# Kernel tuning notes

Measured on AMD Instinct MI355X. Metric: run time of the kernel, lower is better.

## Reference

```python
import jax, jax.numpy as jnp
import numpy as np

N_NODES = 50000
D_MODEL = 128
N_EDGES = 600000
HIDDEN = 128
EDGE_FEAT = 2 * D_MODEL + 2  # 258


def setup_inputs() -> dict:
    key = jax.random.key(0)
    k = jax.random.split(key, 8)
    H = jax.random.normal(k[0], (N_NODES, D_MODEL), dtype=jnp.float32)
    edge_index = jax.random.randint(k[1], (2, N_EDGES), 0, N_NODES, dtype=jnp.int64)
    S_e = jax.random.uniform(k[2], (N_EDGES,), dtype=jnp.float32)
    F_e = jax.random.uniform(k[3], (N_EDGES,), dtype=jnp.float32)
    W1 = jax.random.normal(k[4], (EDGE_FEAT, HIDDEN), dtype=jnp.float32) * (1.0 / np.sqrt(EDGE_FEAT))
    b1 = jnp.zeros((HIDDEN,), dtype=jnp.float32)
    W2 = jax.random.normal(k[5], (HIDDEN, 1), dtype=jnp.float32) * (1.0 / np.sqrt(HIDDEN))
    b2 = jnp.zeros((1,), dtype=jnp.float32)
    return {"H": H, "edge_index": edge_index, "S_e": S_e, "F_e": F_e,
            "W1": W1, "b1": b1, "W2": W2, "b2": b2}


def reference(H, edge_index, S_e, F_e, W1, b1, W2, b2):
    # Gather endpoint node features: [E, D]
    H_u = H[edge_index[0]]
    H_v = H[edge_index[1]]
    H_diff = jnp.abs(H_u - H_v)
    H_prod = H_u * H_v
    # [E, 2D+2]
    edge_features = jnp.concatenate(
        [H_diff, H_prod, S_e[:, None], F_e[:, None]], axis=1)
    # 2-layer MLP with SiLU (dropout is identity in eval mode)
    h = jax.nn.silu(edge_features @ W1 + b1)
    a_e = (h @ W2 + b2)[:, 0]  # [E]
    return a_e
```

## Files before the change

kernel.cpp:

```cpp
#include <hip/hip_runtime.h>


typedef _Float16       half8   __attribute__((ext_vector_type(8)));
typedef _Float16       half4v  __attribute__((ext_vector_type(4)));
typedef unsigned short ushort8 __attribute__((ext_vector_type(8)));
typedef float          f32x4   __attribute__((ext_vector_type(4)));

#define NSEG    8

__device__ __forceinline__ float silu_f(float x) {
    return x / (1.0f + __expf(-x));
}


__global__ __launch_bounds__(256)
void cvt_zero_kernel(const float* __restrict__ H, _Float16* __restrict__ Hh,
                     int n4, int* __restrict__ zp, int nz) {
    int i = blockIdx.x * blockDim.x + threadIdx.x;
    if (i < nz) zp[i] = 0;
    if (i < n4) {
        const float4 f = ((const float4*)H)[i];
        half4v h;
        h[0] = (_Float16)f.x; h[1] = (_Float16)f.y;
        h[2] = (_Float16)f.z; h[3] = (_Float16)f.w;
        ((half4v*)Hh)[i] = h;
    }
}

__device__ __forceinline__ void canon(int u, int v, int& a, int& b) {
    const int sw = (u ^ v) & 1;
    a = sw ? v : u;
    b = sw ? u : v;
}

__global__ __launch_bounds__(256)
void hist_kernel(const int* __restrict__ eidx, int* __restrict__ hist,
                 int E, int ASZ, int BBINS) {
    int e = blockIdx.x * blockDim.x + threadIdx.x;
    if (e < E) {
        int a, b;
        canon(eidx[e], eidx[E + e], a, b);
        atomicAdd(&hist[(a / ASZ) * BBINS + (b >> 3)], 1);
    }
}

__global__ __launch_bounds__(256)
void scan1_kernel(int* __restrict__ hist, int* __restrict__ bsum, int NB) {
    __shared__ int s[256];
    const int t = threadIdx.x;
    const int i = blockIdx.x * 256 + t;
    const int v = (i < NB) ? hist[i] : 0;
    s[t] = v;
    __syncthreads();
    for (int off = 1; off < 256; off <<= 1) {
        const int x = (t >= off) ? s[t - off] : 0;
        __syncthreads();
        s[t] += x;
        __syncthreads();
    }
    if (i < NB) hist[i] = s[t] - v;
    if (t == 255) bsum[blockIdx.x] = s[255];
}

__global__ __launch_bounds__(256)
void scan2_kernel(int* __restrict__ bsum, int nb1,
                  const int* __restrict__ hist, int* __restrict__ vbs,
                  int BBINS, int E) {
    __shared__ int s[256];
    const int t = threadIdx.x;
    const int v = (t < nb1) ? bsum[t] : 0;
    s[t] = v;
    __syncthreads();
    for (int off = 1; off < 256; off <<= 1) {
        const int x = (t >= off) ? s[t - off] : 0;
        __syncthreads();
        s[t] += x;
        __syncthreads();
    }
    if (t < nb1) bsum[t] = s[t] - v;
    __syncthreads();
    if (t < NSEG) {
        const int idx = t * BBINS;
        vbs[t] = hist[idx] + bsum[idx >> 8];
    } else if (t == NSEG) {
        vbs[NSEG] = E;
    }
}

__global__ __launch_bounds__(256)
void scatter_kernel(const int* __restrict__ eidx, const float* __restrict__ Se,
                    const float* __restrict__ Fe, int* __restrict__ ofs,
                    const int* __restrict__ bsum,
                    int4* __restrict__ recs, int E, int ASZ, int BBINS) {
    int e = blockIdx.x * blockDim.x + threadIdx.x;
    if (e < E) {
        int a, b;
        canon(eidx[e], eidx[E + e], a, b);
        const int key = (a / ASZ) * BBINS + (b >> 3);
        const int pos = atomicAdd(&ofs[key], 1) + bsum[key >> 8];
        _Float16 sh = (_Float16)Se[e];
        _Float16 fh = (_Float16)Fe[e];
        unsigned pk = (unsigned)*(unsigned short*)&sh
                    | ((unsigned)*(unsigned short*)&fh << 16);
        recs[pos] = make_int4(a, b, e, (int)pk);
    }
}


__device__ __forceinline__ void stage_w1(const float* __restrict__ W1,
                                         _Float16* __restrict__ w1t, int tid) {
    const int n = tid & 127;
    const int g = tid >> 7;
    #pragma unroll
    for (int i = 0; i < 8; ++i) {
        const int kb = g + (i << 2);
        half8 tmp;
        #pragma unroll
        for (int j = 0; j < 8; ++j) {
            const int kp = (kb << 3) + j;
            const int c  = kp >> 5;
            const int r5 = kp & 31;
            const int qq = r5 >> 3;
            const int jj = r5 & 7;
            const int d  = ((c >> 1) << 5) + (qq << 3) + ((c & 1) << 2) + (jj >> 1);
            const int src = ((jj & 1) << 7) + d;
            tmp[j] = (_Float16)W1[src * 128 + n];
        }
        *(half8*)&w1t[n * 256 + ((kb ^ (n & 7)) << 3)] = tmp;
    }
}


__global__ __launch_bounds__(512, 4)
void edgegate_seg(const _Float16* __restrict__ Hh,
                  const int4*  __restrict__ recs,
                  const int*   __restrict__ vbs,
                  int*         __restrict__ ctr,
                  const float* __restrict__ W1,
                  const float* __restrict__ b1,
                  const float* __restrict__ W2,
                  const float* __restrict__ b2,
                  float*       __restrict__ out)
{
    __shared__ _Float16 w1t[128 * 256];
    __shared__ int tkt[2];
    const int tid = threadIdx.x;
    stage_w1(W1, w1t, tid);

    int xcd;
    asm volatile("s_getreg_b32 %0, hwreg(HW_REG_XCC_ID)" : "=s"(xcd));
    xcd &= (NSEG - 1);

    __syncthreads();

    const int lane = tid & 63;
    const int wave = tid >> 6;
    const int q    = lane >> 4;
    const int cb   = lane & 15;
    const int swz  = cb & 7;

    int p = 0;
    for (int sidx = 0; sidx < NSEG; ++sidx) {
        const int seg = (xcd + sidx) & (NSEG - 1);
        const int vs  = vbs[seg];
        const int ve  = vbs[seg + 1];
        const int ner = ve - vs;
        if (ner <= 0) continue;
        const int Tt = (ner + 255) >> 8;

        while (true) {
            if (tid == 0) tkt[p] = atomicAdd(&ctr[seg], 1);
            __syncthreads();
            const int t0 = tkt[p];
            p ^= 1;
            if (t0 >= Tt) break;

            const int ebase = vs + (t0 << 8) + (wave << 5);

            int a_[2], b_[2], oe_[2];
            float Sf_[2], Ff_[2];
            const _Float16 *up[2], *vp[2];
            #pragma unroll
            for (int g = 0; g < 2; ++g) {
                const int e = min(ebase + (g << 4) + cb, ve - 1);
                const int4 r = recs[e];
                a_[g] = r.x; b_[g] = r.y; oe_[g] = r.z;
                const unsigned pk = (unsigned)r.w;
                const unsigned short sl = (unsigned short)(pk & 0xFFFF);
                const unsigned short fl = (unsigned short)(pk >> 16);
                Sf_[g] = (float)*(const _Float16*)&sl;
                Ff_[g] = (float)*(const _Float16*)&fl;
                up[g] = Hh + (size_t)a_[g] * 128;
                vp[g] = Hh + (size_t)b_[g] * 128;
            }

            f32x4 acc[2][8];
            #pragma unroll
            for (int g = 0; g < 2; ++g)
                #pragma unroll
                for (int t = 0; t < 8; ++t) acc[g][t] = (f32x4){0.f, 0.f, 0.f, 0.f};

            #pragma unroll
            for (int c8 = 0; c8 < 4; ++c8) {
                half8 ae[2], ao[2];
                #pragma unroll
                for (int g = 0; g < 2; ++g) {
                    const half8 u8 = *(const half8*)(up[g] + (c8 << 5) + (q << 3));
                    const half8 v8 = *(const half8*)(vp[g] + (c8 << 5) + (q << 3));
                    half8 d8 = u8 - v8;
                    ushort8 du = *(ushort8*)&d8;
                    du = du & (unsigned short)0x7FFF;
                    const half8 da = *(half8*)&du;
                    const half8 p8 = u8 * v8;
                    ae[g][0]=da[0]; ae[g][1]=p8[0]; ae[g][2]=da[1]; ae[g][3]=p8[1];
                    ae[g][4]=da[2]; ae[g][5]=p8[2]; ae[g][6]=da[3]; ae[g][7]=p8[3];
                    ao[g][0]=da[4]; ao[g][1]=p8[4]; ao[g][2]=da[5]; ao[g][3]=p8[5];
                    ao[g][4]=da[6]; ao[g][5]=p8[6]; ao[g][6]=da[7]; ao[g][7]=p8[7];
                }

                const int kb0 = (((c8 << 1) + 0) * 4 + q) ^ swz;
                const int kb1 = (((c8 << 1) + 1) * 4 + q) ^ swz;
                #pragma unroll
                for (int t = 0; t < 8; ++t) {
                    const half8 b0 = *(const half8*)&w1t[((t << 4) + cb) * 256 + (kb0 << 3)];
                    acc[0][t] = __builtin_amdgcn_mfma_f32_16x16x32_f16(ae[0], b0, acc[0][t], 0, 0, 0);
                    acc[1][t] = __builtin_amdgcn_mfma_f32_16x16x32_f16(ae[1], b0, acc[1][t], 0, 0, 0);
                }
                #pragma unroll
                for (int t = 0; t < 8; ++t) {
                    const half8 b1f = *(const half8*)&w1t[((t << 4) + cb) * 256 + (kb1 << 3)];
                    acc[0][t] = __builtin_amdgcn_mfma_f32_16x16x32_f16(ao[0], b1f, acc[0][t], 0, 0, 0);
                    acc[1][t] = __builtin_amdgcn_mfma_f32_16x16x32_f16(ao[1], b1f, acc[1][t], 0, 0, 0);
                }
            }

            #pragma unroll
            for (int g = 0; g < 2; ++g) {
                float s_r[4], f_r[4]; int oe_r[4];
                #pragma unroll
                for (int rr = 0; rr < 4; ++rr) {
                    const int src = (q << 2) + rr;
                    s_r[rr]  = __shfl(Sf_[g], src);
                    f_r[rr]  = __shfl(Ff_[g], src);
                    oe_r[rr] = __shfl(oe_[g], src);
                }

                float rs[4] = {0.f, 0.f, 0.f, 0.f};
                #pragma unroll
                for (int t = 0; t < 8; ++t) {
                    const int col    = (t << 4) + cb;
                    const float w256 = W1[32768 + col];
                    const float w257 = W1[32896 + col];
                    const float b1c  = b1[col];
                    const float w2c  = W2[col];
                    const f32x4 av = acc[g][t];
                    #pragma unroll
                    for (int rr = 0; rr < 4; ++rr)
                        rs[rr] += silu_f(av[rr] + s_r[rr] * w256 + f_r[rr] * w257 + b1c) * w2c;
                }

                #pragma unroll
                for (int off = 1; off < 16; off <<= 1) {
                    #pragma unroll
                    for (int rr = 0; rr < 4; ++rr) rs[rr] += __shfl_xor(rs[rr], off);
                }

                if (cb == 0) {
                    const float b2v = b2[0];
                    #pragma unroll
                    for (int rr = 0; rr < 4; ++rr) {
                        const int pe = ebase + (g << 4) + (q << 2) + rr;
                        if (pe < ve) out[oe_r[rr]] = rs[rr] + b2v;
                    }
                }
            }
        }
    }
}


__global__ __launch_bounds__(512, 4)
void edgegate_fb(const float* __restrict__ H,
                 const _Float16* __restrict__ Hh,
                 const int*   __restrict__ eidx,
                 const float* __restrict__ Se,
                 const float* __restrict__ Fe,
                 const float* __restrict__ W1,
                 const float* __restrict__ b1,
                 const float* __restrict__ W2,
                 const float* __restrict__ b2,
                 float*       __restrict__ out,
                 int E, int ntiles, int useF16)
{
    __shared__ _Float16 w1t[128 * 256];
    const int tid = threadIdx.x;
    stage_w1(W1, w1t, tid);
    __syncthreads();

    const int lane = tid & 63;
    const int wave = tid >> 6;
    const int q    = lane >> 4;
    const int cb   = lane & 15;
    const int swz  = cb & 7;

    for (int tile = blockIdx.x; tile < ntiles; tile += gridDim.x) {
        const int ebase = tile * 128 + wave * 16;
        int e = ebase + cb;
        if (e >= E) e = E - 1;
        const int u = eidx[e];
        const int v = eidx[E + e];

        f32x4 acc[8];
        #pragma unroll
        for (int t = 0; t < 8; ++t) acc[t] = (f32x4){0.f, 0.f, 0.f, 0.f};

        #pragma unroll
        for (int c8 = 0; c8 < 4; ++c8) {
            half8 ae, ao;
            if (useF16) {
                const _Float16* up = Hh + (size_t)u * 128;
                const _Float16* vp = Hh + (size_t)v * 128;
                const half8 u8 = *(const half8*)(up + (c8 << 5) + (q << 3));
                const half8 v8 = *(const half8*)(vp + (c8 << 5) + (q << 3));
                half8 d8 = u8 - v8;
                ushort8 du = *(ushort8*)&d8;
                du = du & (unsigned short)0x7FFF;
                const half8 da = *(half8*)&du;
                const half8 p8 = u8 * v8;
                ae[0]=da[0]; ae[1]=p8[0]; ae[2]=da[1]; ae[3]=p8[1];
                ae[4]=da[2]; ae[5]=p8[2]; ae[6]=da[3]; ae[7]=p8[3];
                ao[0]=da[4]; ao[1]=p8[4]; ao[2]=da[5]; ao[3]=p8[5];
                ao[4]=da[6]; ao[5]=p8[6]; ao[6]=da[7]; ao[7]=p8[7];
            } else {
                const float* up = H + (size_t)u * 128;
                const float* vp = H + (size_t)v * 128;
                const float4 uu0 = *(const float4*)(up + (c8 << 5) + (q << 3));
                const float4 vv0 = *(const float4*)(vp + (c8 << 5) + (q << 3));
                const float4 uu1 = *(const float4*)(up + (c8 << 5) + (q << 3) + 4);
                const float4 vv1 = *(const float4*)(vp + (c8 << 5) + (q << 3) + 4);
                ae[0]=(_Float16)fabsf(uu0.x-vv0.x); ae[1]=(_Float16)(uu0.x*vv0.x);
                ae[2]=(_Float16)fabsf(uu0.y-vv0.y); ae[3]=(_Float16)(uu0.y*vv0.y);
                ae[4]=(_Float16)fabsf(uu0.z-vv0.z); ae[5]=(_Float16)(uu0.z*vv0.z);
                ae[6]=(_Float16)fabsf(uu0.w-vv0.w); ae[7]=(_Float16)(uu0.w*vv0.w);
                ao[0]=(_Float16)fabsf(uu1.x-vv1.x); ao[1]=(_Float16)(uu1.x*vv1.x);
                ao[2]=(_Float16)fabsf(uu1.y-vv1.y); ao[3]=(_Float16)(uu1.y*vv1.y);
                ao[4]=(_Float16)fabsf(uu1.z-vv1.z); ao[5]=(_Float16)(uu1.z*vv1.z);
                ao[6]=(_Float16)fabsf(uu1.w-vv1.w); ao[7]=(_Float16)(uu1.w*vv1.w);
            }
            const int kb0 = (((c8 << 1) + 0) * 4 + q) ^ swz;
            const int kb1 = (((c8 << 1) + 1) * 4 + q) ^ swz;
            #pragma unroll
            for (int t = 0; t < 8; ++t) {
                const half8 b0 = *(const half8*)&w1t[((t << 4) + cb) * 256 + (kb0 << 3)];
                acc[t] = __builtin_amdgcn_mfma_f32_16x16x32_f16(ae, b0, acc[t], 0, 0, 0);
            }
            #pragma unroll
            for (int t = 0; t < 8; ++t) {
                const half8 b1f = *(const half8*)&w1t[((t << 4) + cb) * 256 + (kb1 << 3)];
                acc[t] = __builtin_amdgcn_mfma_f32_16x16x32_f16(ao, b1f, acc[t], 0, 0, 0);
            }
        }

        const int e0  = ebase + (q << 2);
        const int e0c = (e0 + 3 < E) ? e0 : (E - 4);
        const float4 s4 = *(const float4*)(Se + e0c);
        const float4 f4 = *(const float4*)(Fe + e0c);

        float rs0 = 0.f, rs1 = 0.f, rs2 = 0.f, rs3 = 0.f;
        #pragma unroll
        for (int t = 0; t < 8; ++t) {
            const int col    = (t << 4) + cb;
            const float w256 = W1[32768 + col];
            const float w257 = W1[32896 + col];
            const float b1c  = b1[col];
            const float w2c  = W2[col];
            const f32x4 av = acc[t];
            rs0 += silu_f(av[0] + s4.x * w256 + f4.x * w257 + b1c) * w2c;
            rs1 += silu_f(av[1] + s4.y * w256 + f4.y * w257 + b1c) * w2c;
            rs2 += silu_f(av[2] + s4.z * w256 + f4.z * w257 + b1c) * w2c;
            rs3 += silu_f(av[3] + s4.w * w256 + f4.w * w257 + b1c) * w2c;
        }
        #pragma unroll
        for (int off = 1; off < 16; off <<= 1) {
            rs0 += __shfl_xor(rs0, off);
            rs1 += __shfl_xor(rs1, off);
            rs2 += __shfl_xor(rs2, off);
            rs3 += __shfl_xor(rs3, off);
        }
        if (cb == 0 && e0 < E) {
            const float b2v = b2[0];
            out[e0]     = rs0 + b2v;
            out[e0 + 1] = rs1 + b2v;
            out[e0 + 2] = rs2 + b2v;
            out[e0 + 3] = rs3 + b2v;
        }
    }
}


static inline size_t align256(size_t x) { return (x + 255) & ~(size_t)255; }

extern "C" void kernel_launch(void* const* d_in, const int* in_sizes, int n_in,
                              void* d_out, int out_size, void* d_ws, size_t ws_size,
                              hipStream_t stream)
{
    const float* H    = (const float*)d_in[0];
    const int*   eidx = (const int*)  d_in[1];
    const float* Se   = (const float*)d_in[2];
    const float* Fe   = (const float*)d_in[3];
    const float* W1   = (const float*)d_in[4];
    const float* b1   = (const float*)d_in[5];
    const float* W2   = (const float*)d_in[6];
    const float* b2   = (const float*)d_in[7];
    float* out = (float*)d_out;

    const int nH     = in_sizes[0];
    const int nNodes = nH / 128;
    const int E      = in_sizes[2];
    const int ntiles = (E + 127) / 128;

    const int ASZ   = (nNodes + NSEG - 1) / NSEG;
    const int BBINS = (nNodes + 7) >> 3;
    const int NB    = NSEG * BBINS;
    const int nb1   = (NB + 255) / 256;

    const size_t hhB    = (size_t)nH * sizeof(_Float16);
    const size_t off_g  = align256(hhB);
    const size_t off_bs = align256(off_g + (size_t)(NB + 8) * 4);
    const size_t off_vb = align256(off_bs + 256 * 4);
    const size_t off_r  = align256(off_vb + 16 * 4);
    const size_t need   = off_r + (size_t)E * sizeof(int4);

    if (ws_size >= need && nb1 <= 256) {
        _Float16* Hh   = (_Float16*)((char*)d_ws);
        int*      hist = (int*)     ((char*)d_ws + off_g);
        int*      ctr  = hist + NB;
        int*      bsum = (int*)     ((char*)d_ws + off_bs);
        int*      vbs  = (int*)     ((char*)d_ws + off_vb);
        int4*     recs = (int4*)    ((char*)d_ws + off_r);

        const int n4 = nH / 4;
        hipLaunchKernelGGL(cvt_zero_kernel, dim3((n4 + 255) / 256), dim3(256), 0,
                           stream, H, Hh, n4, hist, NB + 8);
        hipLaunchKernelGGL(hist_kernel, dim3((E + 255) / 256), dim3(256), 0, stream,
                           eidx, hist, E, ASZ, BBINS);
        hipLaunchKernelGGL(scan1_kernel, dim3(nb1), dim3(256), 0, stream,
                           hist, bsum, NB);
        hipLaunchKernelGGL(scan2_kernel, dim3(1), dim3(256), 0, stream,
                           bsum, nb1, hist, vbs, BBINS, E);
        hipLaunchKernelGGL(scatter_kernel, dim3((E + 255) / 256), dim3(256), 0, stream,
                           eidx, Se, Fe, hist, bsum, recs, E, ASZ, BBINS);

        hipLaunchKernelGGL(edgegate_seg, dim3(512), dim3(512), 0, stream,
                           Hh, recs, vbs, ctr, W1, b1, W2, b2, out);
    } else if (ws_size >= hhB) {
        _Float16* Hh = (_Float16*)d_ws;
        const int n4 = nH / 4;
        const int grid = (512 < ntiles) ? 512 : ntiles;
        hipLaunchKernelGGL(cvt_zero_kernel, dim3((n4 + 255) / 256), dim3(256), 0,
                           stream, H, Hh, n4, (int*)nullptr, 0);
        hipLaunchKernelGGL(edgegate_fb, dim3(grid), dim3(512), 0, stream,
                           H, Hh, eidx, Se, Fe, W1, b1, W2, b2, out, E, ntiles, 1);
    } else {
        const int grid = (512 < ntiles) ? 512 : ntiles;
        hipLaunchKernelGGL(edgegate_fb, dim3(grid), dim3(512), 0, stream,
                           H, (const _Float16*)nullptr, eidx, Se, Fe, W1, b1, W2, b2,
                           out, E, ntiles, 0);
    }
}
```

Baseline: 307.4 us.

## Fuse preprocessing and edge MLP into one cooperative megakernel with grid syncs

Replaces the six-kernel pipeline (convert/zero, histogram, two scans, scatter, edge MLP) with a single cooperative kernel that separates the phases with grid.sync, removing the per-launch overhead and the gaps between small kernels. The scan is reworked into a per-block chunk scan plus a block-0 scan of the block sums. The edge tile per wave shrinks from 32 to 16 edges, which lowers register pressure but gives less reuse of W1 fragments. The W1 staging permutation is simplified so the MFMA operands no longer need interleaving shuffles. Grid syncs add their own latency, and the old pipeline remains as a fallback if the cooperative launch fails.

```diff
diff --git a/kernel.cpp b/kernel.cpp
--- a/kernel.cpp
+++ b/kernel.cpp
@@ -1,4 +1,7 @@
 #include <hip/hip_runtime.h>
+#include <hip/hip_cooperative_groups.h>
+
+namespace cg = cooperative_groups;
 
 
 typedef _Float16       half8   __attribute__((ext_vector_type(8)));
@@ -10,6 +13,243 @@
 
 __device__ __forceinline__ float silu_f(float x) {
     return x / (1.0f + __expf(-x));
+}
+
+__device__ __forceinline__ void canon(int u, int v, int& a, int& b) {
+    const int sw = (u ^ v) & 1;
+    a = sw ? v : u;
+    b = sw ? u : v;
+}
+
+
+__device__ __forceinline__ void stage_w1(const float* __restrict__ W1,
+                                         _Float16* __restrict__ w1t, int tid) {
+    const int n = tid & 127;
+    const int g = tid >> 7;
+    #pragma unroll
+    for (int i = 0; i < 8; ++i) {
+        const int kb = g + (i << 2);
+        half8 tmp;
+        #pragma unroll
+        for (int j = 0; j < 8; ++j) {
+            const int kp  = (kb << 3) + j;
+            const int c   = kp >> 5;
+            const int k32 = kp & 31;
+            const int src = ((c & 1) << 7) + ((c >> 1) << 5) + k32;
+            tmp[j] = (_Float16)W1[src * 128 + n];
+        }
+        *(half8*)&w1t[n * 256 + ((kb ^ (n & 7)) << 3)] = tmp;
+    }
+}
+
+
+__device__ __forceinline__ void edge_tile16(
+    const _Float16* __restrict__ Hh, const int4* __restrict__ recs,
+    const _Float16* __restrict__ w1t,
+    const float* __restrict__ W1, const float* __restrict__ b1,
+    const float* __restrict__ W2, float b2v, float* __restrict__ out,
+    int ebase, int elim, int q, int cb, int swz)
+{
+    const int e = min(ebase + cb, elim - 1);
+    const int4 r = recs[e];
+    const int a = r.x, b = r.y, oe = r.z;
+    const unsigned pk = (unsigned)r.w;
+    const unsigned short sl = (unsigned short)(pk & 0xFFFF);
+    const unsigned short fl = (unsigned short)(pk >> 16);
+    const float Sf = (float)*(const _Float16*)&sl;
+    const float Ff = (float)*(const _Float16*)&fl;
+
+    const _Float16* up = Hh + (size_t)a * 128;
+    const _Float16* vp = Hh + (size_t)b * 128;
+
+    f32x4 acc[8];
+    #pragma unroll
+    for (int t = 0; t < 8; ++t) acc[t] = (f32x4){0.f, 0.f, 0.f, 0.f};
+
+    #pragma unroll
+    for (int c8 = 0; c8 < 4; ++c8) {
+        const half8 u8 = *(const half8*)(up + (c8 << 5) + (q << 3));
+        const half8 v8 = *(const half8*)(vp + (c8 << 5) + (q << 3));
+        half8 d8 = u8 - v8;
+        ushort8 du = *(ushort8*)&d8;
+        du = du & (unsigned short)0x7FFF;
+        const half8 ae = *(half8*)&du;
+        const half8 ao = u8 * v8;
+
+        const int kb0 = ((c8 << 3) + q) ^ swz;
+        const int kb1 = ((c8 << 3) + 4 + q) ^ swz;
+        #pragma unroll
+        for (int t = 0; t < 8; ++t) {
+            const half8 b0 = *(const half8*)&w1t[((t << 4) + cb) * 256 + (kb0 << 3)];
+            acc[t] = __builtin_amdgcn_mfma_f32_16x16x32_f16(ae, b0, acc[t], 0, 0, 0);
+        }
+        #pragma unroll
+        for (int t = 0; t < 8; ++t) {
+            const half8 b1f = *(const half8*)&w1t[((t << 4) + cb) * 256 + (kb1 << 3)];
+            acc[t] = __builtin_amdgcn_mfma_f32_16x16x32_f16(ao, b1f, acc[t], 0, 0, 0);
+        }
+    }
+
+    float s_r[4], f_r[4]; int oe_r[4];
+    #pragma unroll
+    for (int rr = 0; rr < 4; ++rr) {
+        const int src = (q << 2) + rr;
+        s_r[rr]  = __shfl(Sf, src);
+        f_r[rr]  = __shfl(Ff, src);
+        oe_r[rr] = __shfl(oe, src);
+    }
+
+    float rs[4] = {0.f, 0.f, 0.f, 0.f};
+    #pragma unroll
+    for (int t = 0; t < 8; ++t) {
+        const int col    = (t << 4) + cb;
+        const float w256 = W1[32768 + col];
+        const float w257 = W1[32896 + col];
+        const float b1c  = b1[col];
+        const float w2c  = W2[col];
+        const f32x4 av = acc[t];
+        #pragma unroll
+        for (int rr = 0; rr < 4; ++rr)
+            rs[rr] += silu_f(av[rr] + s_r[rr] * w256 + f_r[rr] * w257 + b1c) * w2c;
+    }
+
+    #pragma unroll
+    for (int off = 1; off < 16; off <<= 1) {
+        #pragma unroll
+        for (int rr = 0; rr < 4; ++rr) rs[rr] += __shfl_xor(rs[rr], off);
+    }
+
+    if (cb == 0) {
+        #pragma unroll
+        for (int rr = 0; rr < 4; ++rr) {
+            const int pe = ebase + (q << 2) + rr;
+            if (pe < elim) out[oe_r[rr]] = rs[rr] + b2v;
+        }
+    }
+}
+
+
+__global__ __launch_bounds__(512, 4)
+void edgegate_mega(const float* __restrict__ H, _Float16* __restrict__ Hh,
+                   const int* __restrict__ eidx,
+                   const float* __restrict__ Se, const float* __restrict__ Fe,
+                   const float* __restrict__ W1, const float* __restrict__ b1,
+                   const float* __restrict__ W2, const float* __restrict__ b2,
+                   float* __restrict__ out,
+                   int* __restrict__ hist,
+                   int* __restrict__ bsum,
+                   int* __restrict__ vbs,
+                   int4* __restrict__ recs,
+                   int E, int n4, int NB, int ASZ, int BBINS)
+{
+    cg::grid_group grid = cg::this_grid();
+    __shared__ _Float16 w1t[128 * 256];
+    __shared__ int s[512];
+    __shared__ int tkt[2];
+
+    const int tid = threadIdx.x;
+    const int gid = blockIdx.x * blockDim.x + tid;
+    const int G   = gridDim.x * blockDim.x;
+
+    for (int i = gid; i < NB + 8; i += G) hist[i] = 0;
+    for (int i = gid; i < n4; i += G) {
+        const float4 f = ((const float4*)H)[i];
+        half4v h;
+        h[0] = (_Float16)f.x; h[1] = (_Float16)f.y;
+        h[2] = (_Float16)f.z; h[3] = (_Float16)f.w;
+        ((half4v*)Hh)[i] = h;
+    }
+    stage_w1(W1, w1t, tid);
+    grid.sync();
+
+    for (int e = gid; e < E; e += G) {
+        int a, b;
+        canon(eidx[e], eidx[E + e], a, b);
+        atomicAdd(&hist[(a / ASZ) * BBINS + (b >> 3)], 1);
+    }
+    grid.sync();
+
+    const int CH    = (NB + (int)gridDim.x - 1) / (int)gridDim.x;
+    const int myBin = blockIdx.x * CH + tid;
+    const int bval  = (tid < CH && myBin < NB) ? hist[myBin] : 0;
+    s[tid] = bval;
+    __syncthreads();
+    for (int off = 1; off < 512; off <<= 1) {
+        const int x = (tid >= off) ? s[tid - off] : 0;
+        __syncthreads();
+        s[tid] += x;
+        __syncthreads();
+    }
+    const int incl = s[tid];
+    if (tid == 511) bsum[blockIdx.x] = incl;
+    grid.sync();
+
+    if (blockIdx.x == 0) {
+        const int bv = bsum[tid];
+        s[tid] = bv;
+        __syncthreads();
+        for (int off = 1; off < 512; off <<= 1) {
+            const int x = (tid >= off) ? s[tid - off] : 0;
+            __syncthreads();
+            s[tid] += x;
+            __syncthreads();
+        }
+        bsum[tid] = s[tid] - bv;
+    }
+    grid.sync();
+
+    if (tid < CH && myBin < NB) {
+        const int gv = (incl - bval) + bsum[blockIdx.x];
+        hist[myBin] = gv;
+        if (myBin % BBINS == 0) vbs[myBin / BBINS] = gv;
+    }
+    if (gid == 0) vbs[NSEG] = E;
+    grid.sync();
+
+    for (int e = gid; e < E; e += G) {
+        int a, b;
+        canon(eidx[e], eidx[E + e], a, b);
+        const int key = (a / ASZ) * BBINS + (b >> 3);
+        const int pos = atomicAdd(&hist[key], 1);
+        _Float16 sh = (_Float16)Se[e];
+        _Float16 fh = (_Float16)Fe[e];
+        unsigned pk = (unsigned)*(unsigned short*)&sh
+                    | ((unsigned)*(unsigned short*)&fh << 16);
+        recs[pos] = make_int4(a, b, e, (int)pk);
+    }
+    grid.sync();
+
+    int xcd;
+    asm volatile("s_getreg_b32 %0, hwreg(HW_REG_XCC_ID)" : "=s"(xcd));
+    xcd &= (NSEG - 1);
+
+    int* ctr = hist + NB;
+    const int lane = tid & 63;
+    const int wave = tid >> 6;
+    const int q    = lane >> 4;
+    const int cb   = lane & 15;
+    const int swz  = cb & 7;
+    const float b2v = b2[0];
+
+    int p = 0;
+    for (int sidx = 0; sidx < NSEG; ++sidx) {
+        const int seg = (xcd + sidx) & (NSEG - 1);
+        const int vs  = vbs[seg];
+        const int ve  = vbs[seg + 1];
+        const int ner = ve - vs;
+        if (ner <= 0) continue;
+        const int Tt = (ner + 127) >> 7;
+
+        while (true) {
+            if (tid == 0) tkt[p] = atomicAdd(&ctr[seg], 1);
+            __syncthreads();
+            const int t0 = tkt[p];
+            p ^= 1;
+            if (t0 >= Tt) break;
+            const int ebase = vs + (t0 << 7) + (wave << 4);
+            edge_tile16(Hh, recs, w1t, W1, b1, W2, b2v, out, ebase, ve, q, cb, swz);
+        }
+    }
 }
 
 
@@ -25,12 +265,6 @@
         h[2] = (_Float16)f.z; h[3] = (_Float16)f.w;
         ((half4v*)Hh)[i] = h;
     }
-}
-
-__device__ __forceinline__ void canon(int u, int v, int& a, int& b) {
-    const int sw = (u ^ v) & 1;
-    a = sw ? v : u;
-    b = sw ? u : v;
 }
 
 __global__ __launch_bounds__(256)
@@ -107,30 +341,6 @@
 }
 
 
-__device__ __forceinline__ void stage_w1(const float* __restrict__ W1,
-                                         _Float16* __restrict__ w1t, int tid) {
-    const int n = tid & 127;
-    const int g = tid >> 7;
-    #pragma unroll
-    for (int i = 0; i < 8; ++i) {
-        const int kb = g + (i << 2);
-        half8 tmp;
-        #pragma unroll
-        for (int j = 0; j < 8; ++j) {
-            const int kp = (kb << 3) + j;
-            const int c  = kp >> 5;
-            const int r5 = kp & 31;
-            const int qq = r5 >> 3;
-            const int jj = r5 & 7;
-            const int d  = ((c >> 1) << 5) + (qq << 3) + ((c & 1) << 2) + (jj >> 1);
-            const int src = ((jj & 1) << 7) + d;
-            tmp[j] = (_Float16)W1[src * 128 + n];
-        }
-        *(half8*)&w1t[n * 256 + ((kb ^ (n & 7)) << 3)] = tmp;
-    }
-}
-
-
 __global__ __launch_bounds__(512, 4)
 void edgegate_seg(const _Float16* __restrict__ Hh,
                   const int4*  __restrict__ recs,
@@ -158,6 +368,7 @@
     const int q    = lane >> 4;
     const int cb   = lane & 15;
     const int swz  = cb & 7;
+    const float b2v = b2[0];
 
     int p = 0;
     for (int sidx = 0; sidx < NSEG; ++sidx) {
@@ -166,7 +377,7 @@
         const int ve  = vbs[seg + 1];
         const int ner = ve - vs;
         if (ner <= 0) continue;
-        const int Tt = (ner + 255) >> 8;
+        const int Tt = (ner + 127) >> 7;
 
         while (true) {
             if (tid == 0) tkt[p] = atomicAdd(&ctr[seg], 1);
@@ -174,106 +385,8 @@
             const int t0 = tkt[p];
             p ^= 1;
             if (t0 >= Tt) break;
-
-            const int ebase = vs + (t0 << 8) + (wave << 5);
-
-            int a_[2], b_[2], oe_[2];
-            float Sf_[2], Ff_[2];
-            const _Float16 *up[2], *vp[2];
-            #pragma unroll
-            for (int g = 0; g < 2; ++g) {
-                const int e = min(ebase + (g << 4) + cb, ve - 1);
-                const int4 r = recs[e];
-                a_[g] = r.x; b_[g] = r.y; oe_[g] = r.z;
-                const unsigned pk = (unsigned)r.w;
-                const unsigned short sl = (unsigned short)(pk & 0xFFFF);
-                const unsigned short fl = (unsigned short)(pk >> 16);
-                Sf_[g] = (float)*(const _Float16*)&sl;
-                Ff_[g] = (float)*(const _Float16*)&fl;
-                up[g] = Hh + (size_t)a_[g] * 128;
-                vp[g] = Hh + (size_t)b_[g] * 128;
-            }
-
-            f32x4 acc[2][8];
-            #pragma unroll
-            for (int g = 0; g < 2; ++g)
-                #pragma unroll
-                for (int t = 0; t < 8; ++t) acc[g][t] = (f32x4){0.f, 0.f, 0.f, 0.f};
-
-            #pragma unroll
-            for (int c8 = 0; c8 < 4; ++c8) {
-                half8 ae[2], ao[2];
-                #pragma unroll
-                for (int g = 0; g < 2; ++g) {
-                    const half8 u8 = *(const half8*)(up[g] + (c8 << 5) + (q << 3));
-                    const half8 v8 = *(const half8*)(vp[g] + (c8 << 5) + (q << 3));
-                    half8 d8 = u8 - v8;
-                    ushort8 du = *(ushort8*)&d8;
-                    du = du & (unsigned short)0x7FFF;
-                    const half8 da = *(half8*)&du;
-                    const half8 p8 = u8 * v8;
-                    ae[g][0]=da[0]; ae[g][1]=p8[0]; ae[g][2]=da[1]; ae[g][3]=p8[1];
-                    ae[g][4]=da[2]; ae[g][5]=p8[2]; ae[g][6]=da[3]; ae[g][7]=p8[3];
-                    ao[g][0]=da[4]; ao[g][1]=p8[4]; ao[g][2]=da[5]; ao[g][3]=p8[5];
-                    ao[g][4]=da[6]; ao[g][5]=p8[6]; ao[g][6]=da[7]; ao[g][7]=p8[7];
-                }
-
-                const int kb0 = (((c8 << 1) + 0) * 4 + q) ^ swz;
-                const int kb1 = (((c8 << 1) + 1) * 4 + q) ^ swz;
-                #pragma unroll
-                for (int t = 0; t < 8; ++t) {
-                    const half8 b0 = *(const half8*)&w1t[((t << 4) + cb) * 256 + (kb0 << 3)];
-                    acc[0][t] = __builtin_amdgcn_mfma_f32_16x16x32_f16(ae[0], b0, acc[0][t], 0, 0, 0);
-                    acc[1][t] = __builtin_amdgcn_mfma_f32_16x16x32_f16(ae[1], b0, acc[1][t], 0, 0, 0);
-                }
-                #pragma unroll
-                for (int t = 0; t < 8; ++t) {
-                    const half8 b1f = *(const half8*)&w1t[((t << 4) + cb) * 256 + (kb1 << 3)];
-                    acc[0][t] = __builtin_amdgcn_mfma_f32_16x16x32_f16(ao[0], b1f, acc[0][t], 0, 0, 0);
-                    acc[1][t] = __builtin_amdgcn_mfma_f32_16x16x32_f16(ao[1], b1f, acc[1][t], 0, 0, 0);
-                }
-            }
-
-            #pragma unroll
-            for (int g = 0; g < 2; ++g) {
-                float s_r[4], f_r[4]; int oe_r[4];
-                #pragma unroll
-                for (int rr = 0; rr < 4; ++rr) {
-                    const int src = (q << 2) + rr;
-                    s_r[rr]  = __shfl(Sf_[g], src);
-                    f_r[rr]  = __shfl(Ff_[g], src);
-                    oe_r[rr] = __shfl(oe_[g], src);
-                }
-
-                float rs[4] = {0.f, 0.f, 0.f, 0.f};
-                #pragma unroll
-                for (int t = 0; t < 8; ++t) {
-                    const int col    = (t << 4) + cb;
-                    const float w256 = W1[32768 + col];
-                    const float w257 = W1[32896 + col];
-                    const float b1c  = b1[col];
-                    const float w2c  = W2[col];
-                    const f32x4 av = acc[g][t];
-                    #pragma unroll
-                    for (int rr = 0; rr < 4; ++rr)
-                        rs[rr] += silu_f(av[rr] + s_r[rr] * w256 + f_r[rr] * w257 + b1c) * w2c;
-                }
-
-                #pragma unroll
-                for (int off = 1; off < 16; off <<= 1) {
-                    #pragma unroll
-                    for (int rr = 0; rr < 4; ++rr) rs[rr] += __shfl_xor(rs[rr], off);
-                }
-
-                if (cb == 0) {
-                    const float b2v = b2[0];
-                    #pragma unroll
-                    for (int rr = 0; rr < 4; ++rr) {
-                        const int pe = ebase + (g << 4) + (q << 2) + rr;
-                        if (pe < ve) out[oe_r[rr]] = rs[rr] + b2v;
-                    }
-                }
-            }
+            const int ebase = vs + (t0 << 7) + (wave << 4);
+            edge_tile16(Hh, recs, w1t, W1, b1, W2, b2v, out, ebase, ve, q, cb, swz);
         }
     }
 }
@@ -325,30 +438,21 @@
                 half8 d8 = u8 - v8;
                 ushort8 du = *(ushort8*)&d8;
                 du = du & (unsigned short)0x7FFF;
-                const half8 da = *(half8*)&du;
-                const half8 p8 = u8 * v8;
-                ae[0]=da[0]; ae[1]=p8[0]; ae[2]=da[1]; ae[3]=p8[1];
-                ae[4]=da[2]; ae[5]=p8[2]; ae[6]=da[3]; ae[7]=p8[3];
-                ao[0]=da[4]; ao[1]=p8[4]; ao[2]=da[5]; ao[3]=p8[5];
-                ao[4]=da[6]; ao[5]=p8[6]; ao[6]=da[7]; ao[7]=p8[7];
+                ae = *(half8*)&du;
+                ao = u8 * v8;
             } else {
                 const float* up = H + (size_t)u * 128;
                 const float* vp = H + (size_t)v * 128;
-                const float4 uu0 = *(const float4*)(up + (c8 << 5) + (q << 3));
-                const float4 vv0 = *(const float4*)(vp + (c8 << 5) + (q << 3));
-                const float4 uu1 = *(const float4*)(up + (c8 << 5) + (q << 3) + 4);
-                const float4 vv1 = *(const float4*)(vp + (c8 << 5) + (q << 3) + 4);
-                ae[0]=(_Float16)fabsf(uu0.x-vv0.x); ae[1]=(_Float16)(uu0.x*vv0.x);
-                ae[2]=(_Float16)fabsf(uu0.y-vv0.y); ae[3]=(_Float16)(uu0.y*vv0.y);
-                ae[4]=(_Float16)fabsf(uu0.z-vv0.z); ae[5]=(_Float16)(uu0.z*vv0.z);
-                ae[6]=(_Float16)fabsf(uu0.w-vv0.w); ae[7]=(_Float16)(uu0.w*vv0.w);
-                ao[0]=(_Float16)fabsf(uu1.x-vv1.x); ao[1]=(_Float16)(uu1.x*vv1.x);
-                ao[2]=(_Float16)fabsf(uu1.y-vv1.y); ao[3]=(_Float16)(uu1.y*vv1.y);
-                ao[4]=(_Float16)fabsf(uu1.z-vv1.z); ao[5]=(_Float16)(uu1.z*vv1.z);
-                ao[6]=(_Float16)fabsf(uu1.w-vv1.w); ao[7]=(_Float16)(uu1.w*vv1.w);
+                #pragma unroll
+                for (int j = 0; j < 8; ++j) {
+                    const float uu = up[(c8 << 5) + (q << 3) + j];
+                    const float vv = vp[(c8 << 5) + (q << 3) + j];
+                    ae[j] = (_Float16)fabsf(uu - vv);
+                    ao[j] = (_Float16)(uu * vv);
+                }
             }
-            const int kb0 = (((c8 << 1) + 0) * 4 + q) ^ swz;
-            const int kb1 = (((c8 << 1) + 1) * 4 + q) ^ swz;
+            const int kb0 = ((c8 << 3) + q) ^ swz;
+            const int kb1 = ((c8 << 3) + 4 + q) ^ swz;
             #pragma unroll
             for (int t = 0; t < 8; ++t) {
                 const half8 b0 = *(const half8*)&w1t[((t << 4) + cb) * 256 + (kb0 << 3)];
@@ -417,6 +521,7 @@
     const int nH     = in_sizes[0];
     const int nNodes = nH / 128;
     const int E      = in_sizes[2];
+    const int n4     = nH / 4;
     const int ntiles = (E + 127) / 128;
 
     const int ASZ   = (nNodes + NSEG - 1) / NSEG;
@@ -427,7 +532,7 @@
     const size_t hhB    = (size_t)nH * sizeof(_Float16);
     const size_t off_g  = align256(hhB);
     const size_t off_bs = align256(off_g + (size_t)(NB + 8) * 4);
-    const size_t off_vb = align256(off_bs + 256 * 4);
+    const size_t off_vb = align256(off_bs + 512 * 4);
     const size_t off_r  = align256(off_vb + 16 * 4);
     const size_t need   = off_r + (size_t)E * sizeof(int4);
 
@@ -439,26 +544,35 @@
         int*      vbs  = (int*)     ((char*)d_ws + off_vb);
         int4*     recs = (int4*)    ((char*)d_ws + off_r);
 
-        const int n4 = nH / 4;
-        hipLaunchKernelGGL(cvt_zero_kernel, dim3((n4 + 255) / 256), dim3(256), 0,
-                           stream, H, Hh, n4, hist, NB + 8);
-        hipLaunchKernelGGL(hist_kernel, dim3((E + 255) / 256), dim3(256), 0, stream,
-                           eidx, hist, E, ASZ, BBINS);
-        hipLaunchKernelGGL(scan1_kernel, dim3(nb1), dim3(256), 0, stream,
-                           hist, bsum, NB);
-        hipLaunchKernelGGL(scan2_kernel, dim3(1), dim3(256), 0, stream,
-                           bsum, nb1, hist, vbs, BBINS, E);
-        hipLaunchKernelGGL(scatter_kernel, dim3((E + 255) / 256), dim3(256), 0, stream,
-                           eidx, Se, Fe, hist, bsum, recs, E, ASZ, BBINS);
-
-        hipLaunchKernelGGL(edgegate_seg, dim3(512), dim3(512), 0, stream,
-                           Hh, recs, vbs, ctr, W1, b1, W2, b2, out);
+        int E_ = E, n4_ = n4, NB_ = NB, ASZ_ = ASZ, BBINS_ = BBINS;
+        void* args[] = { (void*)&H, (void*)&Hh, (void*)&eidx, (void*)&Se,
+                         (void*)&Fe, (void*)&W1, (void*)&b1, (void*)&W2,
+                         (void*)&b2, (void*)&out, (void*)&hist, (void*)&bsum,
+                         (void*)&vbs, (void*)&recs, (void*)&E_, (void*)&n4_,
+                         (void*)&NB_, (void*)&ASZ_, (void*)&BBINS_ };
+        hipError_t err = hipLaunchCooperativeKernel(
+            (const void*)edgegate_mega, dim3(512), dim3(512), args, 0, stream);
+
+        if (err != hipSuccess) {
+            hipLaunchKernelGGL(cvt_zero_kernel, dim3((n4 + 255) / 256), dim3(256),
+                               0, stream, H, Hh, n4, hist, NB + 8);
+            hipLaunchKernelGGL(hist_kernel, dim3((E + 255) / 256), dim3(256),
+                               0, stream, eidx, hist, E, ASZ, BBINS);
+            hipLaunchKernelGGL(scan1_kernel, dim3(nb1), dim3(256), 0, stream,
+                               hist, bsum, NB);
+            hipLaunchKernelGGL(scan2_kernel, dim3(1), dim3(256), 0, stream,
+                               bsum, nb1, hist, vbs, BBINS, E);
+            hipLaunchKernelGGL(scatter_kernel, dim3((E + 255) / 256), dim3(256),
+                               0, stream, eidx, Se, Fe, hist, bsum, recs,
+                               E, ASZ, BBINS);
+            hipLaunchKernelGGL(edgegate_seg, dim3(512), dim3(512), 0, stream,
+                               Hh, recs, vbs, ctr, W1, b1, W2, b2, out);
+        }
     } else if (ws_size >= hhB) {
         _Float16* Hh = (_Float16*)d_ws;
-        const int n4 = nH / 4;
         const int grid = (512 < ntiles) ? 512 : ntiles;
-        hipLaunchKernelGGL(cvt_zero_kernel, dim3((n4 + 255) / 256), dim3(256), 0,
-                           stream, H, Hh, n4, (int*)nullptr, 0);
+        hipLaunchKernelGGL(cvt_zero_kernel, dim3((n4 + 255) / 256), dim3(256),
+                           0, stream, H, Hh, n4, (int*)nullptr, 0);
         hipLaunchKernelGGL(edgegate_fb, dim3(grid), dim3(512), 0, stream,
                            H, Hh, eidx, Se, Fe, W1, b1, W2, b2, out, E, ntiles, 1);
     } else {
```

Measured after the change: 644.3 us. 110% more time.
